# Optimization experiments

Measured on AMD Instinct MI355X. Metric: run time of the kernel, lower is better.

Reference implementation:

```python
import jax, jax.numpy as jnp
import numpy as np

B, S, D, H = 2, 2048, 512, 8
HD = D // H
DFF = 4 * D
EPS_LN = 1e-5
EPS_ATTN = 1e-8


def layernorm(x, w, b):
    mu = jnp.mean(x, axis=-1, keepdims=True)
    var = jnp.var(x, axis=-1, keepdims=True)
    return (x - mu) * jax.lax.rsqrt(var + EPS_LN) * w + b


def masked_attention(q_src, v_src, wq, bq, wk, bk, wv, bv, wo, bo, M):
    # q_src/v_src: (B,S,D); M: (B,S,S)
    Bs, Ss, _ = q_src.shape
    Q = (q_src @ wq + bq).reshape(Bs, Ss, H, HD)
    K = (q_src @ wk + bk).reshape(Bs, Ss, H, HD)
    V = (v_src @ wv + bv).reshape(Bs, Ss, H, HD)
    scale = HD ** -0.5
    scores = jnp.einsum('bqhd,bkhd->bhqk', Q, K) * scale
    Mh = M[:, None, :, :]                      # (B,1,S,S) broadcast over heads
    scores = scores * Mh
    A = jax.nn.softmax(scores, axis=-1)
    A = A * Mh                                 # re-mask post-softmax
    A = A / (jnp.sum(jnp.abs(A), axis=-1, keepdims=True) + EPS_ATTN)  # L1 renorm
    out = jnp.einsum('bhqk,bkhd->bqhd', A, V).reshape(Bs, Ss, D)
    return out @ wo + bo


def ffn(x, w1, b1, w2, b2):
    h = jax.nn.gelu(x @ w1 + b1, approximate=False)
    return x + (h @ w2 + b2)                   # FeedForward(num_layers=2) includes residual


def setup_inputs() -> dict:
    key = jax.random.key(0)
    ks = iter(jax.random.split(key, 64))
    nrm = lambda shape, s=0.02: jax.random.normal(next(ks), shape, jnp.float32) * s
    d = {
        'gene_emb': jax.random.normal(next(ks), (B, S, D), jnp.float32),
        'expr_emb': jax.random.normal(next(ks), (B, S, D), jnp.float32),
        'M': jax.random.uniform(next(ks), (B, S, S), jnp.float32),
    }
    # gene attention params (weights stored (in,out))
    for p in ['g_wq', 'g_wk', 'g_wv', 'g_wo']:
        d[p] = nrm((D, D))
    for p in ['g_bq', 'g_bk', 'g_bv', 'g_bo']:
        d[p] = jnp.zeros((D,), jnp.float32)
    # expr attention params (fused proj 2D->D)
    d['e_wf'] = nrm((2 * D, D)); d['e_bf'] = jnp.zeros((D,), jnp.float32)
    for p in ['e_wq', 'e_wk', 'e_wv', 'e_wo']:
        d[p] = nrm((D, D))
    for p in ['e_bq', 'e_bk', 'e_bv', 'e_bo']:
        d[p] = jnp.zeros((D,), jnp.float32)
    # layernorms
    for p in ['ln_g1_w', 'ln_g2_w', 'ln_e1_w', 'ln_e2_w']:
        d[p] = jnp.ones((D,), jnp.float32)
    for p in ['ln_g1_b', 'ln_g2_b', 'ln_e1_b', 'ln_e2_b']:
        d[p] = jnp.zeros((D,), jnp.float32)
    # FFNs
    d['fg_w1'] = nrm((D, DFF)); d['fg_b1'] = jnp.zeros((DFF,), jnp.float32)
    d['fg_w2'] = nrm((DFF, D)); d['fg_b2'] = jnp.zeros((D,), jnp.float32)
    d['fe_w1'] = nrm((D, DFF)); d['fe_b1'] = jnp.zeros((DFF,), jnp.float32)
    d['fe_w2'] = nrm((DFF, D)); d['fe_b2'] = jnp.zeros((D,), jnp.float32)
    return d


def reference(gene_emb, expr_emb, M,
              g_wq, g_bq, g_wk, g_bk, g_wv, g_bv, g_wo, g_bo,
              e_wf, e_bf, e_wq, e_bq, e_wk, e_bk, e_wv, e_bv, e_wo, e_bo,
              ln_g1_w, ln_g1_b, ln_g2_w, ln_g2_b,
              ln_e1_w, ln_e1_b, ln_e2_w, ln_e2_b,
              fg_w1, fg_b1, fg_w2, fg_b2,
              fe_w1, fe_b1, fe_w2, fe_b2):
    # ----- gene branch -----
    xg = layernorm(gene_emb, ln_g1_w, ln_g1_b)
    attn_g = masked_attention(xg, xg, g_wq, g_bq, g_wk, g_bk, g_wv, g_bv, g_wo, g_bo, M)
    x = gene_emb + attn_g
    x_ln = layernorm(x, ln_g2_w, ln_g2_b)
    out_gene = x + ffn(x_ln, fg_w1, fg_b1, fg_w2, fg_b2)
    # ----- expression branch -----
    y_n = layernorm(expr_emb, ln_e1_w, ln_e1_b)
    fused = jnp.concatenate([gene_emb, y_n], axis=-1) @ e_wf + e_bf
    attn_e = masked_attention(fused, y_n, e_wq, e_bq, e_wk, e_bk, e_wv, e_bv, e_wo, e_bo, M)
    y = expr_emb + attn_e
    y_ln = layernorm(y, ln_e2_w, ln_e2_b)
    out_expr = y + ffn(y_ln, fe_w1, fe_b1, fe_w2, fe_b2)
    return (out_gene, out_expr)
```

## Files before the change

### kernel.cpp

```cpp
#include <hip/hip_runtime.h>
#include <math.h>

#define S_LEN 2048
#define DMODEL 512
#define NROWS 4096
#define NHEAD 8
#define HDIM 64

typedef __attribute__((ext_vector_type(8))) __bf16 bf16x8;
typedef __attribute__((ext_vector_type(4))) float f32x4;

__device__ inline float bf2f(unsigned short h) {
    unsigned u = ((unsigned)h) << 16;
    return __builtin_bit_cast(float, u);
}
__device__ inline unsigned short f2bf(float f) {
    unsigned u = __builtin_bit_cast(unsigned, f);
    return (unsigned short)((u + 0x7fffu + ((u >> 16) & 1u)) >> 16);
}

__device__ inline void gl_lds16(const unsigned short* g, unsigned short* l) {
    __builtin_amdgcn_global_load_lds(
        (const __attribute__((address_space(1))) void*)g,
        (__attribute__((address_space(3))) void*)l, 16, 0, 0);
}

__global__ __launch_bounds__(256) void wcast_t(
    const float* __restrict__ W, unsigned short* __restrict__ Wt, int K, int Mo)
{
    __shared__ float t[32][33];
    const int bx = blockIdx.x * 32;
    const int by = blockIdx.y * 32;
    const int tx = threadIdx.x & 31, ty = threadIdx.x >> 5;
    #pragma unroll
    for (int r = 0; r < 4; ++r)
        t[ty + 8 * r][tx] = W[(size_t)(by + ty + 8 * r) * Mo + bx + tx];
    __syncthreads();
    #pragma unroll
    for (int r = 0; r < 4; ++r)
        Wt[(size_t)(bx + ty + 8 * r) * K + by + tx] = f2bf(t[tx][ty + 8 * r]);
}

__global__ __launch_bounds__(256) void wcast_sq8(
    const float* w0, const float* w1, const float* w2, const float* w3,
    const float* w4, const float* w5, const float* w6, const float* w7,
    unsigned short* __restrict__ dst)
{
    const float* srcs[8] = {w0, w1, w2, w3, w4, w5, w6, w7};
    const float* __restrict__ W = srcs[blockIdx.z];
    unsigned short* __restrict__ Wt = dst + (size_t)blockIdx.z * 512 * 512;
    __shared__ float t[32][33];
    const int bx = blockIdx.x * 32, by = blockIdx.y * 32;
    const int tx = threadIdx.x & 31, ty = threadIdx.x >> 5;
    #pragma unroll
    for (int r = 0; r < 4; ++r)
        t[ty + 8 * r][tx] = W[(size_t)(by + ty + 8 * r) * 512 + bx + tx];
    __syncthreads();
    #pragma unroll
    for (int r = 0; r < 4; ++r)
        Wt[(size_t)(bx + ty + 8 * r) * 512 + by + tx] = f2bf(t[tx][ty + 8 * r]);
}

__global__ __launch_bounds__(256) void wcast_t2(
    const float* wA, const float* wB, unsigned short* __restrict__ dst,
    int K, int Mo)
{
    const float* __restrict__ W = blockIdx.z ? wB : wA;
    unsigned short* __restrict__ Wt = dst + (size_t)blockIdx.z * K * Mo;
    __shared__ float t[32][33];
    const int bx = blockIdx.x * 32, by = blockIdx.y * 32;
    const int tx = threadIdx.x & 31, ty = threadIdx.x >> 5;
    #pragma unroll
    for (int r = 0; r < 4; ++r)
        t[ty + 8 * r][tx] = W[(size_t)(by + ty + 8 * r) * Mo + bx + tx];
    __syncthreads();
    #pragma unroll
    for (int r = 0; r < 4; ++r)
        Wt[(size_t)(bx + ty + 8 * r) * K + by + tx] = f2bf(t[tx][ty + 8 * r]);
}

__global__ __launch_bounds__(256) void pack_bias(
    const float* __restrict__ b1, const float* __restrict__ b2,
    const float* __restrict__ b3, float* __restrict__ dst, int n)
{
    int t = blockIdx.x * 256 + threadIdx.x;
    if (t >= n) return;
    float v = (t < 512) ? b1[t] : (t < 1024) ? b2[t - 512] : b3[t - 1024];
    dst[t] = v;
}

__global__ __launch_bounds__(256) void cast_strided(
    const float* __restrict__ in, unsigned short* __restrict__ out, int ostride)
{
    const int row = blockIdx.x, t = threadIdx.x;
    out[(size_t)row * ostride + t]       = f2bf(in[(size_t)row * DMODEL + t]);
    out[(size_t)row * ostride + t + 256] = f2bf(in[(size_t)row * DMODEL + t + 256]);
}

__global__ __launch_bounds__(256) void ln_kernel(
    const float* __restrict__ x, const float* __restrict__ w,
    const float* __restrict__ b, unsigned short* __restrict__ y, int ostride)
{
    __shared__ float red[8];
    const int row = blockIdx.x;
    const float* xr = x + (size_t)row * DMODEL;
    const int t = threadIdx.x;
    float v0 = xr[t];
    float v1 = xr[t + 256];
    float s  = v0 + v1;
    float sq = v0 * v0 + v1 * v1;
    #pragma unroll
    for (int o = 32; o > 0; o >>= 1) {
        s  += __shfl_down(s, o);
        sq += __shfl_down(sq, o);
    }
    int wid = t >> 6, lane = t & 63;
    if (lane == 0) { red[wid] = s; red[4 + wid] = sq; }
    __syncthreads();
    float mean = (red[0] + red[1] + red[2] + red[3]) * (1.0f / 512.0f);
    float msq  = (red[4] + red[5] + red[6] + red[7]) * (1.0f / 512.0f);
    float var  = msq - mean * mean;
    float rs   = rsqrtf(var + 1e-5f);
    y[(size_t)row * ostride + t]       = f2bf((v0 - mean) * rs * w[t] + b[t]);
    y[(size_t)row * ostride + t + 256] = f2bf((v1 - mean) * rs * w[t + 256] + b[t + 256]);
}

__global__ __launch_bounds__(256) void vtrans(
    const unsigned short* __restrict__ V, int ldv, unsigned short* __restrict__ Vt)
{
    __shared__ unsigned short t[64][72];
    const int s0 = blockIdx.x * 64, h = blockIdx.y, b = blockIdx.z;
    const int tid = threadIdx.x;
    {
        const int r = tid >> 2, c = (tid & 3) * 16;
        const unsigned short* src = V + (size_t)(b * S_LEN + s0 + r) * ldv + h * 64 + c;
        *(int4*)&t[r][c]     = *(const int4*)(src);
        *(int4*)&t[r][c + 8] = *(const int4*)(src + 8);
    }
    __syncthreads();
    {
        const int d = tid >> 2, s = (tid & 3) * 16;
        unsigned short* dst = Vt + ((size_t)((b * 8 + h) * 64 + d)) * S_LEN + s0 + s;
        unsigned short tmp[16];
        #pragma unroll
        for (int e = 0; e < 16; ++e) tmp[e] = t[s + e][d];
        *(int4*)dst       = *(int4*)&tmp[0];
        *(int4*)(dst + 8) = *(int4*)&tmp[8];
    }
}

__global__ __launch_bounds__(256) void gemm_mfma(
    const unsigned short* __restrict__ A, int lda,
    const unsigned short* __restrict__ Bt,
    const float* __restrict__ bias,
    const float* __restrict__ R1,
    const unsigned short* __restrict__ R2,
    float* __restrict__ Cf, unsigned short* __restrict__ Cb,
    int K, int Mo, int dogelu)
{
    __shared__ __align__(16) unsigned short As[128 * 32];
    __shared__ __align__(16) unsigned short Bs[128 * 32];
    const int tid = threadIdx.x;
    const int wave = tid >> 6, lane = tid & 63;
    const int wr = wave >> 1, wc = wave & 1;
    const int row0 = blockIdx.y * 128, col0 = blockIdx.x * 128;
    const int l15 = lane & 15, q = lane >> 4;

    f32x4 acc[4][4];
    const f32x4 zz = {0.f, 0.f, 0.f, 0.f};
    #pragma unroll
    for (int i = 0; i < 4; ++i)
        #pragma unroll
        for (int j = 0; j < 4; ++j) acc[i][j] = zz;

    for (int k0 = 0; k0 < K; k0 += 32) {
        #pragma unroll
        for (int r = 0; r < 2; ++r) {
            int idx = r * 256 + tid;
            int row = idx >> 2, kc = idx & 3;
            gl_lds16(&A[(size_t)(row0 + row) * lda + k0 + kc * 8],
                     &As[(size_t)(r * 256 + wave * 64) * 8]);
            gl_lds16(&Bt[(size_t)(col0 + row) * K + k0 + kc * 8],
                     &Bs[(size_t)(r * 256 + wave * 64) * 8]);
        }
        __syncthreads();
        bf16x8 af[4], bfr[4];
        #pragma unroll
        for (int fi = 0; fi < 4; ++fi)
            af[fi] = *(const bf16x8*)&As[(wr * 64 + fi * 16 + l15) * 32 + q * 8];
        #pragma unroll
        for (int fj = 0; fj < 4; ++fj)
            bfr[fj] = *(const bf16x8*)&Bs[(wc * 64 + fj * 16 + l15) * 32 + q * 8];
        #pragma unroll
        for (int fi = 0; fi < 4; ++fi)
            #pragma unroll
            for (int fj = 0; fj < 4; ++fj)
                acc[fi][fj] = __builtin_amdgcn_mfma_f32_16x16x32_bf16(
                    af[fi], bfr[fj], acc[fi][fj], 0, 0, 0);
        __syncthreads();
    }

    #pragma unroll
    for (int fi = 0; fi < 4; ++fi) {
        #pragma unroll
        for (int reg = 0; reg < 4; ++reg) {
            int row = row0 + wr * 64 + fi * 16 + q * 4 + reg;
            #pragma unroll
            for (int fj = 0; fj < 4; ++fj) {
                int col = col0 + wc * 64 + fj * 16 + l15;
                float v = acc[fi][fj][reg] + bias[col];
                if (dogelu) v = 0.5f * v * (1.0f + erff(v * 0.70710678118654752f));
                size_t off = (size_t)row * Mo + col;
                if (R1) v += R1[off];
                if (R2) v += bf2f(R2[off]);
                if (Cb) Cb[off] = f2bf(v);
                else    Cf[off] = v;
            }
        }
    }
}

__global__ __launch_bounds__(256) void gemm_mfma64(
    const unsigned short* __restrict__ A, int lda,
    const unsigned short* __restrict__ Bt,
    const float* __restrict__ bias,
    const float* __restrict__ R1,
    const unsigned short* __restrict__ R2,
    float* __restrict__ Cf, unsigned short* __restrict__ Cb,
    int K, int Mo, int dogelu)
{
    __shared__ __align__(16) unsigned short As[64 * 64];
    __shared__ __align__(16) unsigned short Bs[64 * 64];
    const int tid = threadIdx.x;
    const int wave = tid >> 6, lane = tid & 63;
    const int row0 = blockIdx.y * 64, col0 = blockIdx.x * 64;
    const int l15 = lane & 15, q = lane >> 4;

    f32x4 acc[4];
    const f32x4 zz = {0.f, 0.f, 0.f, 0.f};
    #pragma unroll
    for (int j = 0; j < 4; ++j) acc[j] = zz;

    for (int k0 = 0; k0 < K; k0 += 64) {
        #pragma unroll
        for (int r = 0; r < 2; ++r) {
            int idx = r * 256 + tid;
            int row = idx >> 3, kc = idx & 7;
            gl_lds16(&A[(size_t)(row0 + row) * lda + k0 + kc * 8],
                     &As[(size_t)(r * 256 + wave * 64) * 8]);
            gl_lds16(&Bt[(size_t)(col0 + row) * K + k0 + kc * 8],
                     &Bs[(size_t)(r * 256 + wave * 64) * 8]);
        }
        __syncthreads();
        #pragma unroll
        for (int ks = 0; ks < 2; ++ks) {
            bf16x8 af = *(const bf16x8*)&As[(wave * 16 + l15) * 64 + ks * 32 + q * 8];
            bf16x8 bfr[4];
            #pragma unroll
            for (int fj = 0; fj < 4; ++fj)
                bfr[fj] = *(const bf16x8*)&Bs[(fj * 16 + l15) * 64 + ks * 32 + q * 8];
            #pragma unroll
            for (int fj = 0; fj < 4; ++fj)
                acc[fj] = __builtin_amdgcn_mfma_f32_16x16x32_bf16(af, bfr[fj], acc[fj], 0, 0, 0);
        }
        __syncthreads();
    }

    #pragma unroll
    for (int reg = 0; reg < 4; ++reg) {
        int row = row0 + wave * 16 + q * 4 + reg;
        #pragma unroll
        for (int fj = 0; fj < 4; ++fj) {
            int col = col0 + fj * 16 + l15;
            float v = acc[fj][reg] + bias[col];
            if (dogelu) v = 0.5f * v * (1.0f + erff(v * 0.70710678118654752f));
            size_t off = (size_t)row * Mo + col;
            if (R1) v += R1[off];
            if (R2) v += bf2f(R2[off]);
            if (Cb) Cb[off] = f2bf(v);
            else    Cf[off] = v;
        }
    }
}

__global__ __launch_bounds__(256, 4) void attn_mfma_split(
    const unsigned short* __restrict__ Q, int ldq,
    const unsigned short* __restrict__ Kp, int ldk,
    const unsigned short* __restrict__ Vt,
    const float* __restrict__ M,
    unsigned short* __restrict__ Opart,
    float* __restrict__ stats)
{
    __shared__ __align__(16) unsigned short Ks[64 * 72];
    __shared__ __align__(16) unsigned short Vs[64 * 72];
    __shared__ __align__(16) float Ms[4][16 * 68];

    const int bh = blockIdx.y, b = bh >> 3, h = bh & 7;
    const int q0 = blockIdx.x * 64;
    const int p = blockIdx.z;
    const int tid = threadIdx.x, wave = tid >> 6, lane = tid & 63;
    const int l15 = lane & 15, quad = lane >> 4;
    const int iRow = q0 + wave * 16 + l15;
    const int kBeg = p * (S_LEN / 2), kEnd = kBeg + (S_LEN / 2);

    unsigned short* Ps = (unsigned short*)&Ms[wave][0];

    bf16x8 qf[2];
    {
        const unsigned short* qp = Q + (size_t)(b * S_LEN + iRow) * ldq + h * HDIM + quad * 8;
        #pragma unroll
        for (int ks = 0; ks < 2; ++ks) {
            union { bf16x8 v; unsigned short u[8]; } tq;
            tq.v = *(const bf16x8*)(qp + ks * 32);
            #pragma unroll
            for (int e = 0; e < 8; ++e) tq.u[e] = f2bf(bf2f(tq.u[e]) * 0.125f);
            qf[ks] = tq.v;
        }
    }

    float rm = -INFINITY, rZ = 0.f, rZm = 0.f;
    f32x4 oacc[4];
    const f32x4 zz = {0.f, 0.f, 0.f, 0.f};
    #pragma unroll
    for (int dt = 0; dt < 4; ++dt) oacc[dt] = zz;

    const int srow = tid >> 3;
    const int scol = (tid & 7) * 8;
    const unsigned short* kg = Kp + ((size_t)b * S_LEN) * ldk + h * HDIM + scol;
    const unsigned short* vg = Vt + ((size_t)bh * 64 + srow) * S_LEN + scol;
    const float* mg = M + (size_t)b * S_LEN * S_LEN + (size_t)(q0 + wave * 16) * S_LEN;

    for (int k0 = kBeg; k0 < kEnd; k0 += 64) {
        __syncthreads();
        int4 kv0 = *(const int4*)(kg + (size_t)(k0 + srow) * ldk);
        int4 kv1 = *(const int4*)(kg + (size_t)(k0 + srow + 32) * ldk);
        int4 vv0 = *(const int4*)(vg + k0);
        int4 vv1 = *(const int4*)(vg + 32 * S_LEN + k0);
        float4 mv[4];
        #pragma unroll
        for (int c = 0; c < 4; ++c)
            mv[c] = *(const float4*)(mg + (size_t)(c * 4 + quad) * S_LEN + k0 + l15 * 4);
        *(int4*)&Ks[srow * 72 + scol]        = kv0;
        *(int4*)&Ks[(srow + 32) * 72 + scol] = kv1;
        *(int4*)&Vs[srow * 72 + scol]        = vv0;
        *(int4*)&Vs[(srow + 32) * 72 + scol] = vv1;
        #pragma unroll
        for (int c = 0; c < 4; ++c)
            *(float4*)&Ms[wave][(c * 4 + quad) * 68 + l15 * 4] = mv[c];
        __syncthreads();

        float4 m4[4];
        #pragma unroll
        for (int jt = 0; jt < 4; ++jt)
            m4[jt] = *(const float4*)&Ms[wave][l15 * 68 + jt * 16 + quad * 4];

        f32x4 sacc[4];
        #pragma unroll
        for (int jt = 0; jt < 4; ++jt) sacc[jt] = zz;
        #pragma unroll
        for (int jt = 0; jt < 4; ++jt) {
            bf16x8 kf0 = *(const bf16x8*)&Ks[(jt * 16 + l15) * 72 + quad * 8];
            bf16x8 kf1 = *(const bf16x8*)&Ks[(jt * 16 + l15) * 72 + 32 + quad * 8];
            sacc[jt] = __builtin_amdgcn_mfma_f32_16x16x32_bf16(kf0, qf[0], sacc[jt], 0, 0, 0);
            sacc[jt] = __builtin_amdgcn_mfma_f32_16x16x32_bf16(kf1, qf[1], sacc[jt], 0, 0, 0);
        }

        float mx = -INFINITY;
        #pragma unroll
        for (int jt = 0; jt < 4; ++jt) {
            float mm[4] = {m4[jt].x, m4[jt].y, m4[jt].z, m4[jt].w};
            #pragma unroll
            for (int r = 0; r < 4; ++r) {
                sacc[jt][r] = sacc[jt][r] * mm[r];
                mx = fmaxf(mx, sacc[jt][r]);
            }
        }
        mx = fmaxf(mx, __shfl_xor(mx, 16));
        mx = fmaxf(mx, __shfl_xor(mx, 32));
        float mn = fmaxf(rm, mx);
        float al = __expf(rm - mn);
        rm = mn; rZ *= al; rZm *= al;
        #pragma unroll
        for (int dt = 0; dt < 4; ++dt)
            #pragma unroll
            for (int r = 0; r < 4; ++r) oacc[dt][r] *= al;

        float z = 0.f, zm = 0.f;
        #pragma unroll
        for (int jt = 0; jt < 4; ++jt) {
            float mm[4] = {m4[jt].x, m4[jt].y, m4[jt].z, m4[jt].w};
            float pv[4];
            #pragma unroll
            for (int r = 0; r < 4; ++r) {
                float e = __expf(sacc[jt][r] - mn);
                float pm = e * mm[r];
                z += e; zm += pm; pv[r] = pm;
            }
            unsigned lo = (unsigned)f2bf(pv[0]) | ((unsigned)f2bf(pv[1]) << 16);
            unsigned hi = (unsigned)f2bf(pv[2]) | ((unsigned)f2bf(pv[3]) << 16);
            uint2 pk; pk.x = lo; pk.y = hi;
            *(uint2*)&Ps[l15 * 72 + jt * 16 + quad * 4] = pk;
        }
        z  += __shfl_xor(z, 16);  z  += __shfl_xor(z, 32);
        zm += __shfl_xor(zm, 16); zm += __shfl_xor(zm, 32);
        rZ += z; rZm += zm;

        bf16x8 pf0 = *(const bf16x8*)&Ps[l15 * 72 + quad * 8];
        bf16x8 pf1 = *(const bf16x8*)&Ps[l15 * 72 + 32 + quad * 8];
        #pragma unroll
        for (int dt = 0; dt < 4; ++dt) {
            bf16x8 vf0 = *(const bf16x8*)&Vs[(dt * 16 + l15) * 72 + quad * 8];
            bf16x8 vf1 = *(const bf16x8*)&Vs[(dt * 16 + l15) * 72 + 32 + quad * 8];
            oacc[dt] = __builtin_amdgcn_mfma_f32_16x16x32_bf16(vf0, pf0, oacc[dt], 0, 0, 0);
            oacc[dt] = __builtin_amdgcn_mfma_f32_16x16x32_bf16(vf1, pf1, oacc[dt], 0, 0, 0);
        }
    }

    unsigned short* op = Opart + (((size_t)(p * 16 + bh) * S_LEN + iRow) * 64);
    #pragma unroll
    for (int dt = 0; dt < 4; ++dt) {
        ushort4 o4;
        o4.x = f2bf(oacc[dt][0]); o4.y = f2bf(oacc[dt][1]);
        o4.z = f2bf(oacc[dt][2]); o4.w = f2bf(oacc[dt][3]);
        *(ushort4*)(op + dt * 16 + quad * 4) = o4;
    }
    if (quad == 0) {
        float4 st; st.x = rm; st.y = rZ; st.z = rZm; st.w = 0.f;
        *(float4*)&stats[(((size_t)p * 16 + bh) * S_LEN + iRow) * 4] = st;
    }
}

__global__ __launch_bounds__(256) void attn_combine(
    const unsigned short* __restrict__ Opart, const float* __restrict__ stats,
    unsigned short* __restrict__ O)
{
    const int bh = blockIdx.y, b = bh >> 3, h = bh & 7;
    const int q0 = blockIdx.x * 64;
    const int tid = threadIdx.x;
    const int i = tid >> 2, dq = (tid & 3) * 16;
    const int qg = q0 + i;

    float4 s0 = *(const float4*)&stats[(((size_t)0 * 16 + bh) * S_LEN + qg) * 4];
    float4 s1 = *(const float4*)&stats[(((size_t)1 * 16 + bh) * S_LEN + qg) * 4];
    float ms = fmaxf(s0.x, s1.x);
    float w0 = __expf(s0.x - ms), w1 = __expf(s1.x - ms);
    float Z  = w0 * s0.y + w1 * s1.y;
    float Zm = w0 * s0.z + w1 * s1.z;
    float inv = 1.0f / (Zm + 1e-8f * Z);
    w0 *= inv; w1 *= inv;

    const unsigned short* p0 = Opart + (((size_t)0 * 16 + bh) * S_LEN + qg) * 64 + dq;
    const unsigned short* p1 = Opart + (((size_t)1 * 16 + bh) * S_LEN + qg) * 64 + dq;
    union { int4 v; unsigned short u[8]; } a0, a1, r;
    unsigned short* dst = O + (size_t)(b * S_LEN + qg) * DMODEL + h * HDIM + dq;
    #pragma unroll
    for (int half = 0; half < 2; ++half) {
        a0.v = *(const int4*)(p0 + half * 8);
        a1.v = *(const int4*)(p1 + half * 8);
        #pragma unroll
        for (int e = 0; e < 8; ++e)
            r.u[e] = f2bf(w0 * bf2f(a0.u[e]) + w1 * bf2f(a1.u[e]));
        *(int4*)(dst + half * 8) = r.v;
    }
}

extern "C" void kernel_launch(void* const* d_in, const int* in_sizes, int n_in,
                              void* d_out, int out_size, void* d_ws, size_t ws_size,
                              hipStream_t stream)
{
    const float* gene_emb = (const float*)d_in[0];
    const float* expr_emb = (const float*)d_in[1];
    const float* M        = (const float*)d_in[2];
    const float* g_wq = (const float*)d_in[3];
    const float* g_wk = (const float*)d_in[4];
    const float* g_wv = (const float*)d_in[5];
    const float* g_wo = (const float*)d_in[6];
    const float* g_bq = (const float*)d_in[7];
    const float* g_bk = (const float*)d_in[8];
    const float* g_bv = (const float*)d_in[9];
    const float* g_bo = (const float*)d_in[10];
    const float* e_wf = (const float*)d_in[11];
    const float* e_bf = (const float*)d_in[12];
    const float* e_wq = (const float*)d_in[13];
    const float* e_wk = (const float*)d_in[14];
    const float* e_wv = (const float*)d_in[15];
    const float* e_wo = (const float*)d_in[16];
    const float* e_bq = (const float*)d_in[17];
    const float* e_bk = (const float*)d_in[18];
    const float* e_bv = (const float*)d_in[19];
    const float* e_bo = (const float*)d_in[20];
    const float* ln_g1_w = (const float*)d_in[21];
    const float* ln_g2_w = (const float*)d_in[22];
    const float* ln_e1_w = (const float*)d_in[23];
    const float* ln_e2_w = (const float*)d_in[24];
    const float* ln_g1_b = (const float*)d_in[25];
    const float* ln_g2_b = (const float*)d_in[26];
    const float* ln_e1_b = (const float*)d_in[27];
    const float* ln_e2_b = (const float*)d_in[28];
    const float* fg_w1 = (const float*)d_in[29];
    const float* fg_b1 = (const float*)d_in[30];
    const float* fg_w2 = (const float*)d_in[31];
    const float* fg_b2 = (const float*)d_in[32];
    const float* fe_w1 = (const float*)d_in[33];
    const float* fe_b1 = (const float*)d_in[34];
    const float* fe_w2 = (const float*)d_in[35];
    const float* fe_b2 = (const float*)d_in[36];

    float* out_gene = (float*)d_out;
    float* out_expr = out_gene + (size_t)NROWS * DMODEL;

    char* ws = (char*)d_ws;
    const size_t MB1 = 1024 * 1024;
    unsigned short* bufA16  = (unsigned short*)(ws + 0 * MB1);
    unsigned short* bufAt16 = (unsigned short*)(ws + 4 * MB1);
    unsigned short* bufQKV  = (unsigned short*)(ws + 8 * MB1);
    unsigned short* bufQKe  = (unsigned short*)(ws + 8 * MB1);
    unsigned short* bufV16  = (unsigned short*)(ws + 16 * MB1);
    unsigned short* bufVt   = (unsigned short*)(ws + 20 * MB1);
    unsigned short* bufCat  = (unsigned short*)(ws + 24 * MB1);
    unsigned short* bufOp   = (unsigned short*)(ws + 24 * MB1);
    float*          bufSt   = (float*)(ws + 32 * MB1);
    float*          bufX    = (float*)(ws + 33 * MB1);
    unsigned short* bufH16  = (unsigned short*)(ws + 8 * MB1);
    char* wp = ws + 41 * MB1;
    unsigned short* sq8    = (unsigned short*)wp;
    unsigned short* gwq_t  = sq8 + 0 * 512 * 512;
    unsigned short* gwk_t  = sq8 + 1 * 512 * 512;
    unsigned short* gwv_t  = sq8 + 2 * 512 * 512;
    unsigned short* gwo_t  = sq8 + 3 * 512 * 512;
    unsigned short* ewq_t  = sq8 + 4 * 512 * 512;
    unsigned short* ewk_t  = sq8 + 5 * 512 * 512;
    unsigned short* ewv_t  = sq8 + 6 * 512 * 512;
    unsigned short* ewo_t  = sq8 + 7 * 512 * 512;
    unsigned short* ewf_t  = sq8 + 8 * 512 * 512;
    unsigned short* ffn1   = ewf_t + 1024 * 512;
    unsigned short* fgw1_t = ffn1;
    unsigned short* few1_t = ffn1 + 512 * 2048;
    unsigned short* ffn2   = few1_t + 512 * 2048;
    unsigned short* fgw2_t = ffn2;
    unsigned short* few2_t = ffn2 + 2048 * 512;
    float* biasg = (float*)(few2_t + 2048 * 512);
    float* biase = biasg + 1536;

    dim3 blk(256);
    dim3 ln_grid(NROWS);
    dim3 g512s(8, 64);
    dim3 g1024(8, 32);
    dim3 g1536(12, 32);
    dim3 g2048(16, 32);
    dim3 attn_grid(S_LEN / 64, 16, 2);
    dim3 comb_grid(S_LEN / 64, 16);
    dim3 vt_grid(S_LEN / 64, NHEAD, 2);

    wcast_sq8<<<dim3(16, 16, 8), blk, 0, stream>>>(
        g_wq, g_wk, g_wv, g_wo, e_wq, e_wk, e_wv, e_wo, sq8);
    wcast_t<<<dim3(16, 32), blk, 0, stream>>>(e_wf, ewf_t, 1024, 512);
    wcast_t2<<<dim3(64, 16, 2), blk, 0, stream>>>(fg_w1, fe_w1, ffn1, 512, 2048);
    wcast_t2<<<dim3(16, 64, 2), blk, 0, stream>>>(fg_w2, fe_w2, ffn2, 2048, 512);
    pack_bias<<<dim3(6), blk, 0, stream>>>(g_bq, g_bk, g_bv, biasg, 1536);
    pack_bias<<<dim3(4), blk, 0, stream>>>(e_bq, e_bk, e_bk, biase, 1024);

    ln_kernel<<<ln_grid, blk, 0, stream>>>(gene_emb, ln_g1_w, ln_g1_b, bufA16, 512);
    gemm_mfma<<<g1536, blk, 0, stream>>>(bufA16, 512, gwq_t, biasg, nullptr, nullptr, nullptr, bufQKV, 512, 1536, 0);
    vtrans<<<vt_grid, blk, 0, stream>>>(bufQKV + 1024, 1536, bufVt);
    attn_mfma_split<<<attn_grid, blk, 0, stream>>>(bufQKV, 1536, bufQKV + 512, 1536, bufVt, M, bufOp, bufSt);
    attn_combine<<<comb_grid, blk, 0, stream>>>(bufOp, bufSt, bufAt16);
    gemm_mfma64<<<g512s, blk, 0, stream>>>(bufAt16, 512, gwo_t, g_bo, gene_emb, nullptr, bufX, nullptr, 512, 512, 0);
    ln_kernel<<<ln_grid, blk, 0, stream>>>(bufX, ln_g2_w, ln_g2_b, bufA16, 512);
    gemm_mfma<<<g2048, blk, 0, stream>>>(bufA16, 512, fgw1_t, fg_b1, nullptr, nullptr, nullptr, bufH16, 512, 2048, 1);
    gemm_mfma64<<<g512s, blk, 0, stream>>>(bufH16, 2048, fgw2_t, fg_b2, bufX, bufA16, out_gene, nullptr, 2048, 512, 0);

    cast_strided<<<ln_grid, blk, 0, stream>>>(gene_emb, bufCat, 1024);
    ln_kernel<<<ln_grid, blk, 0, stream>>>(expr_emb, ln_e1_w, ln_e1_b, bufCat + 512, 1024);
    gemm_mfma64<<<g512s, blk, 0, stream>>>(bufCat, 1024, ewf_t, e_bf, nullptr, nullptr, nullptr, bufA16, 1024, 512, 0);
    gemm_mfma<<<g1024, blk, 0, stream>>>(bufA16, 512, ewq_t, biase, nullptr, nullptr, nullptr, bufQKe, 512, 1024, 0);
    gemm_mfma64<<<g512s, blk, 0, stream>>>(bufCat + 512, 1024, ewv_t, e_bv, nullptr, nullptr, nullptr, bufV16, 512, 512, 0);
    vtrans<<<vt_grid, blk, 0, stream>>>(bufV16, 512, bufVt);
    attn_mfma_split<<<attn_grid, blk, 0, stream>>>(bufQKe, 1024, bufQKe + 512, 1024, bufVt, M, bufOp, bufSt);
    attn_combine<<<comb_grid, blk, 0, stream>>>(bufOp, bufSt, bufAt16);
    gemm_mfma64<<<g512s, blk, 0, stream>>>(bufAt16, 512, ewo_t, e_bo, expr_emb, nullptr, bufX, nullptr, 512, 512, 0);
    ln_kernel<<<ln_grid, blk, 0, stream>>>(bufX, ln_e2_w, ln_e2_b, bufA16, 512);
    gemm_mfma<<<g2048, blk, 0, stream>>>(bufA16, 512, few1_t, fe_b1, nullptr, nullptr, nullptr, bufH16, 512, 2048, 1);
    gemm_mfma64<<<g512s, blk, 0, stream>>>(bufH16, 2048, few2_t, fe_b2, bufX, bufA16, out_expr, nullptr, 2048, 512, 0);
}
```

Measured before the change: 547.0 us.

## Load K/V/mask tiles directly from global in attention, use exp2 softmax

The split attention kernel no longer stages K, V and mask tiles through shared memory behind block barriers. Each wave now reads its MFMA operands and mask values straight from global memory, and the key loop is unrolled by two to give more loads in flight. Softmax switches to exp2, with log2e folded into the Q prescale and the combine kernel updated to match. Float-to-bf16 packing uses v_cvt_pk_bf16_f32, and MFMA sections are wrapped in s_setprio. The cost is that all four waves redundantly fetch the same K/V tiles through the cache, and global load latency is no longer hidden by a shared-memory stage.

```diff
diff --git a/kernel.cpp b/kernel.cpp
--- a/kernel.cpp
+++ b/kernel.cpp
@@ -6,6 +6,7 @@
 #define NROWS 4096
 #define NHEAD 8
 #define HDIM 64
+#define LOG2E 1.4426950408889634f
 
 typedef __attribute__((ext_vector_type(8))) __bf16 bf16x8;
 typedef __attribute__((ext_vector_type(4))) float f32x4;
@@ -291,9 +292,7 @@
     unsigned short* __restrict__ Opart,
     float* __restrict__ stats)
 {
-    __shared__ __align__(16) unsigned short Ks[64 * 72];
-    __shared__ __align__(16) unsigned short Vs[64 * 72];
-    __shared__ __align__(16) float Ms[4][16 * 68];
+    __shared__ __align__(16) unsigned short Ps_all[4][16 * 72];
 
     const int bh = blockIdx.y, b = bh >> 3, h = bh & 7;
     const int q0 = blockIdx.x * 64;
@@ -303,7 +302,7 @@
     const int iRow = q0 + wave * 16 + l15;
     const int kBeg = p * (S_LEN / 2), kEnd = kBeg + (S_LEN / 2);
 
-    unsigned short* Ps = (unsigned short*)&Ms[wave][0];
+    unsigned short* Ps = &Ps_all[wave][0];
 
     bf16x8 qf[2];
     {
@@ -313,10 +312,15 @@
             union { bf16x8 v; unsigned short u[8]; } tq;
             tq.v = *(const bf16x8*)(qp + ks * 32);
             #pragma unroll
-            for (int e = 0; e < 8; ++e) tq.u[e] = f2bf(bf2f(tq.u[e]) * 0.125f);
+            for (int e = 0; e < 8; ++e)
+                tq.u[e] = f2bf(bf2f(tq.u[e]) * (0.125f * LOG2E));
             qf[ks] = tq.v;
         }
     }
+
+    const unsigned short* kl = Kp + ((size_t)b * S_LEN + l15) * ldk + h * HDIM + quad * 8;
+    const unsigned short* vl = Vt + ((size_t)bh * 64 + l15) * S_LEN + quad * 8;
+    const float*        mrow = M + ((size_t)b * S_LEN + iRow) * S_LEN + quad * 4;
 
     float rm = -INFINITY, rZ = 0.f, rZm = 0.f;
     f32x4 oacc[4];
@@ -324,46 +328,26 @@
     #pragma unroll
     for (int dt = 0; dt < 4; ++dt) oacc[dt] = zz;
 
-    const int srow = tid >> 3;
-    const int scol = (tid & 7) * 8;
-    const unsigned short* kg = Kp + ((size_t)b * S_LEN) * ldk + h * HDIM + scol;
-    const unsigned short* vg = Vt + ((size_t)bh * 64 + srow) * S_LEN + scol;
-    const float* mg = M + (size_t)b * S_LEN * S_LEN + (size_t)(q0 + wave * 16) * S_LEN;
-
+    #pragma unroll 2
     for (int k0 = kBeg; k0 < kEnd; k0 += 64) {
-        __syncthreads();
-        int4 kv0 = *(const int4*)(kg + (size_t)(k0 + srow) * ldk);
-        int4 kv1 = *(const int4*)(kg + (size_t)(k0 + srow + 32) * ldk);
-        int4 vv0 = *(const int4*)(vg + k0);
-        int4 vv1 = *(const int4*)(vg + 32 * S_LEN + k0);
-        float4 mv[4];
-        #pragma unroll
-        for (int c = 0; c < 4; ++c)
-            mv[c] = *(const float4*)(mg + (size_t)(c * 4 + quad) * S_LEN + k0 + l15 * 4);
-        *(int4*)&Ks[srow * 72 + scol]        = kv0;
-        *(int4*)&Ks[(srow + 32) * 72 + scol] = kv1;
-        *(int4*)&Vs[srow * 72 + scol]        = vv0;
-        *(int4*)&Vs[(srow + 32) * 72 + scol] = vv1;
-        #pragma unroll
-        for (int c = 0; c < 4; ++c)
-            *(float4*)&Ms[wave][(c * 4 + quad) * 68 + l15 * 4] = mv[c];
-        __syncthreads();
-
         float4 m4[4];
         #pragma unroll
         for (int jt = 0; jt < 4; ++jt)
-            m4[jt] = *(const float4*)&Ms[wave][l15 * 68 + jt * 16 + quad * 4];
+            m4[jt] = *(const float4*)(mrow + k0 + jt * 16);
 
         f32x4 sacc[4];
         #pragma unroll
         for (int jt = 0; jt < 4; ++jt) sacc[jt] = zz;
+        __builtin_amdgcn_s_setprio(1);
         #pragma unroll
         for (int jt = 0; jt < 4; ++jt) {
-            bf16x8 kf0 = *(const bf16x8*)&Ks[(jt * 16 + l15) * 72 + quad * 8];
-            bf16x8 kf1 = *(const bf16x8*)&Ks[(jt * 16 + l15) * 72 + 32 + quad * 8];
+            const unsigned short* kr = kl + (size_t)((k0 + jt * 16) * ldk);
+            bf16x8 kf0 = *(const bf16x8*)(kr);
+            bf16x8 kf1 = *(const bf16x8*)(kr + 32);
             sacc[jt] = __builtin_amdgcn_mfma_f32_16x16x32_bf16(kf0, qf[0], sacc[jt], 0, 0, 0);
             sacc[jt] = __builtin_amdgcn_mfma_f32_16x16x32_bf16(kf1, qf[1], sacc[jt], 0, 0, 0);
         }
+        __builtin_amdgcn_s_setprio(0);
 
         float mx = -INFINITY;
         #pragma unroll
@@ -378,7 +362,7 @@
         mx = fmaxf(mx, __shfl_xor(mx, 16));
         mx = fmaxf(mx, __shfl_xor(mx, 32));
         float mn = fmaxf(rm, mx);
-        float al = __expf(rm - mn);
+        float al = __builtin_amdgcn_exp2f(rm - mn);
         rm = mn; rZ *= al; rZm *= al;
         #pragma unroll
         for (int dt = 0; dt < 4; ++dt)
@@ -392,12 +376,13 @@
             float pv[4];
             #pragma unroll
             for (int r = 0; r < 4; ++r) {
-                float e = __expf(sacc[jt][r] - mn);
+                float e = __builtin_amdgcn_exp2f(sacc[jt][r] - mn);
                 float pm = e * mm[r];
                 z += e; zm += pm; pv[r] = pm;
             }
-            unsigned lo = (unsigned)f2bf(pv[0]) | ((unsigned)f2bf(pv[1]) << 16);
-            unsigned hi = (unsigned)f2bf(pv[2]) | ((unsigned)f2bf(pv[3]) << 16);
+            unsigned lo, hi;
+            asm("v_cvt_pk_bf16_f32 %0, %1, %2" : "=v"(lo) : "v"(pv[0]), "v"(pv[1]));
+            asm("v_cvt_pk_bf16_f32 %0, %1, %2" : "=v"(hi) : "v"(pv[2]), "v"(pv[3]));
             uint2 pk; pk.x = lo; pk.y = hi;
             *(uint2*)&Ps[l15 * 72 + jt * 16 + quad * 4] = pk;
         }
@@ -407,22 +392,26 @@
 
         bf16x8 pf0 = *(const bf16x8*)&Ps[l15 * 72 + quad * 8];
         bf16x8 pf1 = *(const bf16x8*)&Ps[l15 * 72 + 32 + quad * 8];
+        __builtin_amdgcn_s_setprio(1);
         #pragma unroll
         for (int dt = 0; dt < 4; ++dt) {
-            bf16x8 vf0 = *(const bf16x8*)&Vs[(dt * 16 + l15) * 72 + quad * 8];
-            bf16x8 vf1 = *(const bf16x8*)&Vs[(dt * 16 + l15) * 72 + 32 + quad * 8];
+            const unsigned short* vr = vl + (size_t)(dt * 16) * S_LEN + k0;
+            bf16x8 vf0 = *(const bf16x8*)(vr);
+            bf16x8 vf1 = *(const bf16x8*)(vr + 32);
             oacc[dt] = __builtin_amdgcn_mfma_f32_16x16x32_bf16(vf0, pf0, oacc[dt], 0, 0, 0);
             oacc[dt] = __builtin_amdgcn_mfma_f32_16x16x32_bf16(vf1, pf1, oacc[dt], 0, 0, 0);
         }
+        __builtin_amdgcn_s_setprio(0);
     }
 
     unsigned short* op = Opart + (((size_t)(p * 16 + bh) * S_LEN + iRow) * 64);
     #pragma unroll
     for (int dt = 0; dt < 4; ++dt) {
-        ushort4 o4;
-        o4.x = f2bf(oacc[dt][0]); o4.y = f2bf(oacc[dt][1]);
-        o4.z = f2bf(oacc[dt][2]); o4.w = f2bf(oacc[dt][3]);
-        *(ushort4*)(op + dt * 16 + quad * 4) = o4;
+        unsigned lo, hi;
+        asm("v_cvt_pk_bf16_f32 %0, %1, %2" : "=v"(lo) : "v"(oacc[dt][0]), "v"(oacc[dt][1]));
+        asm("v_cvt_pk_bf16_f32 %0, %1, %2" : "=v"(hi) : "v"(oacc[dt][2]), "v"(oacc[dt][3]));
+        uint2 o2; o2.x = lo; o2.y = hi;
+        *(uint2*)(op + dt * 16 + quad * 4) = o2;
     }
     if (quad == 0) {
         float4 st; st.x = rm; st.y = rZ; st.z = rZm; st.w = 0.f;
@@ -443,7 +432,7 @@
     float4 s0 = *(const float4*)&stats[(((size_t)0 * 16 + bh) * S_LEN + qg) * 4];
     float4 s1 = *(const float4*)&stats[(((size_t)1 * 16 + bh) * S_LEN + qg) * 4];
     float ms = fmaxf(s0.x, s1.x);
-    float w0 = __expf(s0.x - ms), w1 = __expf(s1.x - ms);
+    float w0 = __builtin_amdgcn_exp2f(s0.x - ms), w1 = __builtin_amdgcn_exp2f(s1.x - ms);
     float Z  = w0 * s0.y + w1 * s1.y;
     float Zm = w0 * s0.z + w1 * s1.z;
     float inv = 1.0f / (Zm + 1e-8f * Z);
```

New measurement: 729.9 us. 33.4% more time.
